# Optimization experiments

Hardware: AMD Instinct MI355X
Metric: run time of the kernel (lower is better)

## Reference

```python
import jax, jax.numpy as jnp
import numpy as np

H, W = 16, 16
DIM = 512
HEADS = 8
DIM_HEAD = 64
INNER = HEADS * DIM_HEAD  # 512
B = 8
N = H * W  # 256
SCALE = DIM_HEAD ** -0.5
EPS = 1e-5


def _index_map(h, w):
    # index_map[n, m] = dx * (2w-1) + dy with dx = x-i+h-1, dy = y-j+w-1
    xs = np.arange(h)
    ys = np.arange(w)
    dx = xs[:, None] - xs[None, :] + h - 1            # (h, h)
    dy = ys[:, None] - ys[None, :] + w - 1            # (w, w)
    idx = dx[:, None, :, None] * (2 * w - 1) + dy[None, :, None, :]  # (h, w, h, w)
    return idx.reshape(h * w, h * w).astype(np.int32)


def setup_inputs() -> dict:
    key = jax.random.key(0)
    ks = jax.random.split(key, 5)
    x = jax.random.normal(ks[0], (B, N, DIM), dtype=jnp.float32)
    ln_g = jnp.ones((DIM,), jnp.float32)
    ln_b = jnp.zeros((DIM,), jnp.float32)
    w_qkv = jax.random.normal(ks[1], (DIM, 3 * INNER), jnp.float32) * 0.02
    unique_params = jax.random.normal(ks[2], ((2 * H - 1) * (2 * W - 1), INNER), jnp.float32) * 0.02
    w_out = jax.random.normal(ks[3], (INNER, DIM), jnp.float32) * 0.02
    b_out = jnp.zeros((DIM,), jnp.float32)
    idx_map = jnp.asarray(_index_map(H, W))  # (N, N) int32
    return {"x": x, "ln_g": ln_g, "ln_b": ln_b, "w_qkv": w_qkv,
            "unique_params": unique_params, "w_out": w_out, "b_out": b_out,
            "idx_map": idx_map}


def reference(x, ln_g, ln_b, w_qkv, unique_params, w_out, b_out, idx_map):
    b, n, _ = x.shape
    # LayerNorm
    mu = jnp.mean(x, axis=-1, keepdims=True)
    var = jnp.mean(jnp.square(x - mu), axis=-1, keepdims=True)
    xn = (x - mu) * jax.lax.rsqrt(var + EPS) * ln_g + ln_b
    # qkv projection (no bias)
    qkv = xn @ w_qkv                                  # (b, n, 3*inner)
    q, k, v = jnp.split(qkv, 3, axis=-1)
    q = q.reshape(b, n, HEADS, DIM_HEAD)
    k = k.reshape(b, n, HEADS, DIM_HEAD)
    v = v.reshape(b, n, HEADS, DIM_HEAD)
    # attention scores
    dots = jnp.einsum('bnhd,bmhd->bhnm', q, k) * SCALE
    attn = jax.nn.softmax(dots, axis=-1)              # (b, h, n, m)
    # relative-position table: (n, m, h, d)
    rpos = unique_params[idx_map].reshape(n, n, HEADS, DIM_HEAD)
    # out[b,h,n,d] = sum_m attn[b,h,n,m] * (v[b,m,h,d] + rpos[n,m,h,d])
    out = jnp.einsum('bhnm,bmhd->bnhd', attn, v) \
        + jnp.einsum('bhnm,nmhd->bnhd', attn, rpos)
    out = out.reshape(b, n, INNER)
    return out @ w_out + b_out
```

## Files before the change

kernel.cpp:

```cpp
#include <hip/hip_runtime.h>
#include <math.h>

#define NB 8
#define SEQ 256
#define DIMC 512
#define NHEAD 8
#define DHEAD 64
#define SCALEF 0.125f

typedef __attribute__((ext_vector_type(8))) short s16x8;
typedef __attribute__((ext_vector_type(4))) float f32x4;

typedef __attribute__((address_space(3))) unsigned int lds_u32_t;
typedef const __attribute__((address_space(1))) unsigned int g_u32_t;
static __device__ __forceinline__ void gl_lds16(const void* gsrc, void* ldst) {
  __builtin_amdgcn_global_load_lds((g_u32_t*)gsrc, (lds_u32_t*)ldst, 16, 0, 0);
}

static __device__ __forceinline__ unsigned short f2bf(float f) {
  union { float f; unsigned u; } c; c.f = f;
  unsigned r = c.u + 0x7FFF + ((c.u >> 16) & 1);
  return (unsigned short)(r >> 16);
}
static __device__ __forceinline__ float bf2f(unsigned short u) {
  union { unsigned u; float f; } c; c.u = ((unsigned)u) << 16;
  return c.f;
}

static __device__ void tcast_body(const float* __restrict__ W,
    unsigned short* __restrict__ WT, int K, int N, int n0, int k0, int t,
    float (*tile)[65]) {
#pragma unroll
  for (int i = 0; i < 16; ++i) {
    const int idx = i * 256 + t;
    const int kl = idx >> 6, nl = idx & 63;
    tile[kl][nl] = W[(size_t)(k0 + kl) * N + n0 + nl];
  }
  __syncthreads();
#pragma unroll
  for (int i = 0; i < 16; ++i) {
    const int idx = i * 256 + t;
    const int nl = idx >> 6, kl = idx & 63;
    WT[(size_t)(n0 + nl) * K + k0 + kl] = f2bf(tile[kl][nl]);
  }
}

__global__ __launch_bounds__(256) void prep_kernel(const float* __restrict__ x,
    const float* __restrict__ g, const float* __restrict__ bta,
    const float* __restrict__ w_qkv, const float* __restrict__ w_out,
    const float* __restrict__ up, unsigned short* __restrict__ xnb,
    unsigned short* __restrict__ wqt, unsigned short* __restrict__ wot,
    unsigned short* __restrict__ upb) {
  __shared__ float tile[64][65];
  __shared__ float sh_s[4], sh_q[4];
  const int t = threadIdx.x;
  const int bid = blockIdx.x;
  if (bid < 192) {
    tcast_body(w_qkv, wqt, 512, 1536, (bid % 24) * 64, (bid / 24) * 64, t, tile);
  } else if (bid < 256) {
    const int b2 = bid - 192;
    tcast_body(w_out, wot, 512, 512, (b2 % 8) * 64, (b2 / 8) * 64, t, tile);
  } else if (bid < 497) {
    const int base = (bid - 256) * 2048 + t * 4;
#pragma unroll
    for (int it = 0; it < 2; ++it) {
      const int i = base + it * 1024;
      if (i < 492032) {
        const float4 v = *(const float4*)&up[i];
        ushort4 w;
        w.x = f2bf(v.x); w.y = f2bf(v.y); w.z = f2bf(v.z); w.w = f2bf(v.w);
        *(ushort4*)&upb[i] = w;
      }
    }
  } else {
    const int row = bid - 497;
    const float2 v = ((const float2*)(x + (size_t)row * DIMC))[t];
    float s = v.x + v.y;
    float q = v.x * v.x + v.y * v.y;
#pragma unroll
    for (int off = 32; off > 0; off >>= 1) {
      s += __shfl_down(s, off);
      q += __shfl_down(q, off);
    }
    const int wave = t >> 6, lane = t & 63;
    if (lane == 0) { sh_s[wave] = s; sh_q[wave] = q; }
    __syncthreads();
    const float fs = sh_s[0] + sh_s[1] + sh_s[2] + sh_s[3];
    const float fq = sh_q[0] + sh_q[1] + sh_q[2] + sh_q[3];
    const float mean = fs * (1.0f / DIMC);
    const float inv = rsqrtf(fq * (1.0f / DIMC) - mean * mean + 1e-5f);
    const float2 gv = ((const float2*)g)[t];
    const float2 bv = ((const float2*)bta)[t];
    ushort2 o;
    o.x = f2bf((v.x - mean) * inv * gv.x + bv.x);
    o.y = f2bf((v.y - mean) * inv * gv.y + bv.y);
    ((ushort2*)(xnb + (size_t)row * DIMC))[t] = o;
  }
}

template <int BM, int BN, bool BIAS, bool OUTBF, bool VSPLIT>
__global__ __launch_bounds__(256) void mfma_gemm_bt(
    const unsigned short* __restrict__ A, const unsigned short* __restrict__ BT,
    const float* __restrict__ bias, void* __restrict__ Cv,
    unsigned short* __restrict__ vtb, int M, int K, int N) {
  constexpr int TR = BM / 32;
  constexpr int TC = BN / 32;
  __shared__ unsigned short As[BM * 32];
  __shared__ unsigned short Bs[BN * 32];
  const int t = threadIdx.x;
  const int wave = t >> 6, lane = t & 63;
  const int wr = wave >> 1, wc = wave & 1;
  const int bm = blockIdx.x * BM, bn = blockIdx.y * BN;

  f32x4 acc[TR][TC] = {};

  const int fr = lane & 15, q4 = lane >> 4;
  const int kBlocks = K >> 5;
  for (int kb = 0; kb < kBlocks; ++kb) {
    const int k0 = kb << 5;
    __syncthreads();
#pragma unroll
    for (int c = 0; c < (BM * 4 + 255) / 256; ++c) {
      const int p = c * 256 + t;
      if (BM * 4 % 256 == 0 || p < BM * 4) {
        const int row = p >> 2;
        const int jl = (p & 3) ^ ((row >> 1) & 3);
        gl_lds16(A + (size_t)(bm + row) * K + k0 + jl * 8,
                 As + (size_t)(c * 256 + wave * 64) * 8);
      }
    }
#pragma unroll
    for (int c = 0; c < (BN * 4 + 255) / 256; ++c) {
      const int p = c * 256 + t;
      if (BN * 4 % 256 == 0 || p < BN * 4) {
        const int row = p >> 2;
        const int jl = (p & 3) ^ ((row >> 1) & 3);
        gl_lds16(BT + (size_t)(bn + row) * K + k0 + jl * 8,
                 Bs + (size_t)(c * 256 + wave * 64) * 8);
      }
    }
    __syncthreads();
    s16x8 af[TR], bfr[TC];
#pragma unroll
    for (int i = 0; i < TR; ++i) {
      const int row = wr * (BM / 2) + i * 16 + fr;
      const int jp = q4 ^ ((row >> 1) & 3);
      af[i] = *(const s16x8*)(As + row * 32 + jp * 8);
    }
#pragma unroll
    for (int j = 0; j < TC; ++j) {
      const int row = wc * (BN / 2) + j * 16 + fr;
      const int jp = q4 ^ ((row >> 1) & 3);
      bfr[j] = *(const s16x8*)(Bs + row * 32 + jp * 8);
    }
#pragma unroll
    for (int i = 0; i < TR; ++i)
#pragma unroll
      for (int j = 0; j < TC; ++j)
        acc[i][j] = __builtin_amdgcn_mfma_f32_16x16x32_bf16(af[i], bfr[j],
                                                            acc[i][j], 0, 0, 0);
  }
  if (VSPLIT && bn >= 1024) {
#pragma unroll
    for (int i = 0; i < TR; ++i) {
#pragma unroll
      for (int j = 0; j < TC; ++j) {
        const int hc = bn - 1024 + wc * (BN / 2) + j * 16 + fr;
        const int h = hc >> 6, d = hc & 63;
#pragma unroll
        for (int r = 0; r < 4; ++r) {
          const int row = bm + wr * (BM / 2) + i * 16 + q4 * 4 + r;
          const int b = row >> 8, m = row & 255;
          vtb[(size_t)((b * 8 + h) * 64 + d) * 256 + m] = f2bf(acc[i][j][r]);
        }
      }
    }
    return;
  }
#pragma unroll
  for (int i = 0; i < TR; ++i) {
#pragma unroll
    for (int j = 0; j < TC; ++j) {
      const int col = bn + wc * (BN / 2) + j * 16 + fr;
      const float bv = BIAS ? bias[col] : 0.0f;
#pragma unroll
      for (int r = 0; r < 4; ++r) {
        const int row = bm + wr * (BM / 2) + i * 16 + q4 * 4 + r;
        if constexpr (OUTBF) {
          ((unsigned short*)Cv)[(size_t)row * N + col] = f2bf(acc[i][j][r] + bv);
        } else {
          ((float*)Cv)[(size_t)row * N + col] = acc[i][j][r] + bv;
        }
      }
    }
  }
}

#define PSTR 264
#define KSTR 72
__global__ __launch_bounds__(128) void fused_attn_kernel(
    const unsigned short* __restrict__ qkvb, const unsigned short* __restrict__ vtb,
    unsigned short* __restrict__ attnb, unsigned short* __restrict__ oav) {
  __shared__ unsigned short kv_lds[256 * KSTR];
  __shared__ unsigned short p_lds[32 * PSTR];
  const int bh = blockIdx.y, b = bh >> 3, h = bh & 7;
  const int n0 = blockIdx.x * 32;
  const int t = threadIdx.x, wave = t >> 6, lane = t & 63;
  const int fr = lane & 15, q4 = lane >> 4;

#pragma unroll
  for (int p = 0; p < 16; ++p) {
    const int chunk = p * 128 + t;
    const int m = chunk >> 3, c = chunk & 7;
    *(s16x8*)(kv_lds + m * KSTR + c * 8) =
        *(const s16x8*)(qkvb + (size_t)(b * SEQ + m) * 1536 + 512 + h * 64 + c * 8);
  }
  s16x8 qf[2];
  {
    const size_t qrow = (size_t)(b * SEQ + n0 + wave * 16 + fr) * 1536 + h * 64;
#pragma unroll
    for (int ks = 0; ks < 2; ++ks)
      qf[ks] = *(const s16x8*)(qkvb + qrow + ks * 32 + q4 * 8);
  }
  __syncthreads();

  f32x4 s[16];
#pragma unroll
  for (int mt = 0; mt < 16; ++mt) s[mt] = (f32x4){0.f, 0.f, 0.f, 0.f};
#pragma unroll
  for (int ks = 0; ks < 2; ++ks)
#pragma unroll
    for (int mt = 0; mt < 16; ++mt) {
      const s16x8 kf =
          *(const s16x8*)(kv_lds + (mt * 16 + fr) * KSTR + ks * 32 + q4 * 8);
      s[mt] = __builtin_amdgcn_mfma_f32_16x16x32_bf16(qf[ks], kf, s[mt], 0, 0, 0);
    }

  float mx[4] = {-1e30f, -1e30f, -1e30f, -1e30f};
#pragma unroll
  for (int mt = 0; mt < 16; ++mt)
#pragma unroll
    for (int r = 0; r < 4; ++r) {
      s[mt][r] *= SCALEF;
      mx[r] = fmaxf(mx[r], s[mt][r]);
    }
#pragma unroll
  for (int r = 0; r < 4; ++r) {
    mx[r] = fmaxf(mx[r], __shfl_xor(mx[r], 1));
    mx[r] = fmaxf(mx[r], __shfl_xor(mx[r], 2));
    mx[r] = fmaxf(mx[r], __shfl_xor(mx[r], 4));
    mx[r] = fmaxf(mx[r], __shfl_xor(mx[r], 8));
  }
  float sum[4] = {0.f, 0.f, 0.f, 0.f};
#pragma unroll
  for (int mt = 0; mt < 16; ++mt)
#pragma unroll
    for (int r = 0; r < 4; ++r) {
      s[mt][r] = __expf(s[mt][r] - mx[r]);
      sum[r] += s[mt][r];
    }
#pragma unroll
  for (int r = 0; r < 4; ++r) {
    sum[r] += __shfl_xor(sum[r], 1);
    sum[r] += __shfl_xor(sum[r], 2);
    sum[r] += __shfl_xor(sum[r], 4);
    sum[r] += __shfl_xor(sum[r], 8);
  }
  const float invs[4] = {1.0f / sum[0], 1.0f / sum[1], 1.0f / sum[2],
                         1.0f / sum[3]};

  __syncthreads();

  {
    const int nb = wave * 16 + q4 * 4;
#pragma unroll
    for (int mt = 0; mt < 16; ++mt)
#pragma unroll
      for (int r = 0; r < 4; ++r)
        p_lds[(nb + r) * PSTR + mt * 16 + fr] = f2bf(s[mt][r] * invs[r]);
  }
#pragma unroll
  for (int p = 0; p < 16; ++p) {
    const int idx = p * 128 + t;
    const int d = idx >> 5, c = idx & 31;
    *(s16x8*)(kv_lds + d * PSTR + c * 8) =
        *(const s16x8*)(vtb + (size_t)(bh * 64 + d) * 256 + c * 8);
  }
  __syncthreads();

#pragma unroll
  for (int p = 0; p < 8; ++p) {
    const int idx = p * 128 + t;
    const int row = idx >> 5, mc = (idx & 31) * 8;
    *(s16x8*)(attnb + (size_t)(bh * SEQ + n0 + row) * SEQ + mc) =
        *(const s16x8*)(p_lds + row * PSTR + mc);
  }

  f32x4 o[4];
#pragma unroll
  for (int dt = 0; dt < 4; ++dt) o[dt] = (f32x4){0.f, 0.f, 0.f, 0.f};
#pragma unroll
  for (int ks = 0; ks < 8; ++ks) {
    const s16x8 pf =
        *(const s16x8*)(p_lds + (wave * 16 + fr) * PSTR + ks * 32 + q4 * 8);
#pragma unroll
    for (int dt = 0; dt < 4; ++dt) {
      const s16x8 vf =
          *(const s16x8*)(kv_lds + (dt * 16 + fr) * PSTR + ks * 32 + q4 * 8);
      o[dt] = __builtin_amdgcn_mfma_f32_16x16x32_bf16(pf, vf, o[dt], 0, 0, 0);
    }
  }
#pragma unroll
  for (int dt = 0; dt < 4; ++dt)
#pragma unroll
    for (int r = 0; r < 4; ++r) {
      const int n = n0 + wave * 16 + q4 * 4 + r;
      oav[(size_t)(b * SEQ + n) * DIMC + h * 64 + dt * 16 + fr] = f2bf(o[dt][r]);
    }
}

#define RSTRIDE 280
__global__ __launch_bounds__(256) void rpos_kernel(
    const unsigned short* __restrict__ attnb, const unsigned short* __restrict__ upb,
    unsigned short* __restrict__ ob) {
  __shared__ float aS[4][4 * RSTRIDE];
  const int t = threadIdx.x;
  const int wave = t >> 6, lane = t & 63;
  const int g = lane >> 4, dg = lane & 15;
  const int idx = blockIdx.x * 4 + wave;
  const int bhalf = idx & 1;
  const int h = (idx >> 1) & 7;
  const int n = idx >> 4;
  float* aW = aS[wave];

  const int m4 = lane * 4;
  const int sm4 = m4 + ((m4 >> 6) << 3);
#pragma unroll
  for (int bl = 0; bl < 4; ++bl) {
    const int b = bhalf * 4 + bl;
    const ushort4 v =
        *(const ushort4*)&attnb[(size_t)((b * 8 + h) * SEQ + n) * SEQ + m4];
    float4 f;
    f.x = bf2f(v.x); f.y = bf2f(v.y); f.z = bf2f(v.z); f.w = bf2f(v.w);
    *(float4*)&aW[bl * RSTRIDE + sm4] = f;
  }
  __syncthreads();

  const int xn = n >> 4, yn = n & 15;
  float acc[4][4];
#pragma unroll
  for (int bl = 0; bl < 4; ++bl)
#pragma unroll
    for (int j = 0; j < 4; ++j) acc[bl][j] = 0.0f;

  const int mbase = g * 64;
  const int sbase = g * 72;
#pragma unroll 4
  for (int mm = 0; mm < 64; ++mm) {
    const int m = mbase + mm;
    const int xm = m >> 4, ym = m & 15;
    const int row = (xn - xm + 15) * 31 + (yn - ym + 15);
    const ushort4 uu = *(const ushort4*)&upb[(size_t)row * DIMC + h * 64 + dg * 4];
    const float ux = bf2f(uu.x), uy = bf2f(uu.y), uz = bf2f(uu.z), uw = bf2f(uu.w);
    float ab[4];
#pragma unroll
    for (int bl = 0; bl < 4; ++bl) ab[bl] = aW[bl * RSTRIDE + sbase + mm];
#pragma unroll
    for (int bl = 0; bl < 4; ++bl) {
      acc[bl][0] += ab[bl] * ux;
      acc[bl][1] += ab[bl] * uy;
      acc[bl][2] += ab[bl] * uz;
      acc[bl][3] += ab[bl] * uw;
    }
  }
#pragma unroll
  for (int bl = 0; bl < 4; ++bl)
#pragma unroll
    for (int j = 0; j < 4; ++j) {
      float v = acc[bl][j];
      v += __shfl_xor(v, 16);
      v += __shfl_xor(v, 32);
      acc[bl][j] = v;
    }
  {
    const int b = bhalf * 4 + g;
    const size_t base = (size_t)(b * SEQ + n) * DIMC + h * 64 + dg * 4;
    ushort4 pv = *(ushort4*)&ob[base];
    ushort4 w;
    w.x = f2bf(bf2f(pv.x) + acc[g][0]);
    w.y = f2bf(bf2f(pv.y) + acc[g][1]);
    w.z = f2bf(bf2f(pv.z) + acc[g][2]);
    w.w = f2bf(bf2f(pv.w) + acc[g][3]);
    *(ushort4*)&ob[base] = w;
  }
}

extern "C" void kernel_launch(void* const* d_in, const int* in_sizes, int n_in,
                              void* d_out, int out_size, void* d_ws,
                              size_t ws_size, hipStream_t stream) {
  const float* x = (const float*)d_in[0];
  const float* ln_g = (const float*)d_in[1];
  const float* ln_b = (const float*)d_in[2];
  const float* w_qkv = (const float*)d_in[3];
  const float* up = (const float*)d_in[4];
  const float* w_out = (const float*)d_in[5];
  const float* b_out = (const float*)d_in[6];
  float* out = (float*)d_out;

  unsigned short* u = (unsigned short*)d_ws;
  unsigned short* qkvb = u;
  unsigned short* attnb = u + 3145728;
  unsigned short* xnb = u + 7340032;
  unsigned short* ob = u + 8388608;
  unsigned short* wqt = u + 9437184;
  unsigned short* wot = u + 10223616;
  unsigned short* upb = u + 10485760;
  unsigned short* vtb = u + 10977792;
  if (ws_size < (size_t)12026368 * sizeof(unsigned short)) return;

  prep_kernel<<<2545, 256, 0, stream>>>(x, ln_g, ln_b, w_qkv, w_out, up,
                                        xnb, wqt, wot, upb);
  mfma_gemm_bt<64, 64, false, true, true>
      <<<dim3(32, 24), 256, 0, stream>>>(xnb, wqt, nullptr, qkvb, vtb,
                                         2048, 512, 1536);
  fused_attn_kernel<<<dim3(8, 64), 128, 0, stream>>>(qkvb, vtb, attnb, ob);
  rpos_kernel<<<1024, 256, 0, stream>>>(attnb, upb, ob);
  mfma_gemm_bt<64, 32, true, false, false>
      <<<dim3(32, 16), 256, 0, stream>>>(ob, wot, b_out, out, nullptr,
                                         2048, 512, 512);
}
```

Before: 120.5 us.

## Use K=64 GEMM tiles, move w_out/up casts into QKV GEMM tail, widen rpos loads

The GEMM kernel now stages 64-wide K slices with an 8-way XOR swizzle and issues two MFMA k-steps per barrier pair, which halves the number of sync iterations. The w_out transpose-cast and the unique_params bf16 cast move out of the prep kernel into extra tail blocks of the QKV GEMM launch, so they overlap with GEMM work and the prep kernel gets shorter. The rpos kernel loads 8 bf16 values per lane instead of 4, splitting m across 8 groups and adding one more shuffle-reduction step. The costs are more LDS per GEMM block and extra reduction shuffles in rpos.

New measurement: 120.7 us. Within noise of the previous version (+0.2%).

```diff
diff --git a/kernel.cpp b/kernel.cpp
--- a/kernel.cpp
+++ b/kernel.cpp
@@ -47,33 +47,16 @@
 
 __global__ __launch_bounds__(256) void prep_kernel(const float* __restrict__ x,
     const float* __restrict__ g, const float* __restrict__ bta,
-    const float* __restrict__ w_qkv, const float* __restrict__ w_out,
-    const float* __restrict__ up, unsigned short* __restrict__ xnb,
-    unsigned short* __restrict__ wqt, unsigned short* __restrict__ wot,
-    unsigned short* __restrict__ upb) {
+    const float* __restrict__ w_qkv, unsigned short* __restrict__ xnb,
+    unsigned short* __restrict__ wqt) {
   __shared__ float tile[64][65];
   __shared__ float sh_s[4], sh_q[4];
   const int t = threadIdx.x;
   const int bid = blockIdx.x;
   if (bid < 192) {
     tcast_body(w_qkv, wqt, 512, 1536, (bid % 24) * 64, (bid / 24) * 64, t, tile);
-  } else if (bid < 256) {
-    const int b2 = bid - 192;
-    tcast_body(w_out, wot, 512, 512, (b2 % 8) * 64, (b2 / 8) * 64, t, tile);
-  } else if (bid < 497) {
-    const int base = (bid - 256) * 2048 + t * 4;
-#pragma unroll
-    for (int it = 0; it < 2; ++it) {
-      const int i = base + it * 1024;
-      if (i < 492032) {
-        const float4 v = *(const float4*)&up[i];
-        ushort4 w;
-        w.x = f2bf(v.x); w.y = f2bf(v.y); w.z = f2bf(v.z); w.w = f2bf(v.w);
-        *(ushort4*)&upb[i] = w;
-      }
-    }
   } else {
-    const int row = bid - 497;
+    const int row = bid - 192;
     const float2 v = ((const float2*)(x + (size_t)row * DIMC))[t];
     float s = v.x + v.y;
     float q = v.x * v.x + v.y * v.y;
@@ -98,67 +81,100 @@
   }
 }
 
-template <int BM, int BN, bool BIAS, bool OUTBF, bool VSPLIT>
-__global__ __launch_bounds__(256) void mfma_gemm_bt(
+template <int BM, int BN, bool BIAS, bool OUTBF, bool VSPLIT, bool TAIL>
+__global__ __launch_bounds__(256) void gemm64_kernel(
     const unsigned short* __restrict__ A, const unsigned short* __restrict__ BT,
     const float* __restrict__ bias, void* __restrict__ Cv,
-    unsigned short* __restrict__ vtb, int M, int K, int N) {
+    unsigned short* __restrict__ vtb, int M, int K, int N, int nbm,
+    const float* __restrict__ w_out, unsigned short* __restrict__ wot,
+    const float* __restrict__ up, unsigned short* __restrict__ upb) {
+  constexpr int ABYTES = (BM * 64 + BN * 64) * 2;
+  constexpr int LDSZ = TAIL ? (ABYTES > 16640 ? ABYTES : 16640) : ABYTES;
+  __shared__ alignas(16) unsigned char smem[LDSZ];
+  unsigned short* As = (unsigned short*)smem;
+  unsigned short* Bs = As + BM * 64;
+  const int t = threadIdx.x;
+  const int bid = blockIdx.x;
+  const int gemmBlocks = nbm * (N / BN);
+
+  if constexpr (TAIL) {
+    if (bid >= gemmBlocks) {
+      const int b2 = bid - gemmBlocks;
+      if (b2 < 64) {
+        float (*tile)[65] = (float(*)[65])smem;
+        tcast_body(w_out, wot, 512, 512, (b2 % 8) * 64, (b2 / 8) * 64, t, tile);
+      } else {
+        const int base = (b2 - 64) * 2048 + t * 4;
+#pragma unroll
+        for (int it = 0; it < 2; ++it) {
+          const int i = base + it * 1024;
+          if (i < 492032) {
+            const float4 v = *(const float4*)&up[i];
+            ushort4 w;
+            w.x = f2bf(v.x); w.y = f2bf(v.y); w.z = f2bf(v.z); w.w = f2bf(v.w);
+            *(ushort4*)&upb[i] = w;
+          }
+        }
+      }
+      return;
+    }
+  }
+
   constexpr int TR = BM / 32;
   constexpr int TC = BN / 32;
-  __shared__ unsigned short As[BM * 32];
-  __shared__ unsigned short Bs[BN * 32];
-  const int t = threadIdx.x;
   const int wave = t >> 6, lane = t & 63;
   const int wr = wave >> 1, wc = wave & 1;
-  const int bm = blockIdx.x * BM, bn = blockIdx.y * BN;
+  const int bm = (bid % nbm) * BM, bn = (bid / nbm) * BN;
+  const int fr = lane & 15, q4 = lane >> 4;
 
   f32x4 acc[TR][TC] = {};
 
-  const int fr = lane & 15, q4 = lane >> 4;
-  const int kBlocks = K >> 5;
+  const int kBlocks = K >> 6;
   for (int kb = 0; kb < kBlocks; ++kb) {
-    const int k0 = kb << 5;
+    const int k0 = kb << 6;
     __syncthreads();
 #pragma unroll
-    for (int c = 0; c < (BM * 4 + 255) / 256; ++c) {
+    for (int c = 0; c < BM * 8 / 256; ++c) {
       const int p = c * 256 + t;
-      if (BM * 4 % 256 == 0 || p < BM * 4) {
-        const int row = p >> 2;
-        const int jl = (p & 3) ^ ((row >> 1) & 3);
-        gl_lds16(A + (size_t)(bm + row) * K + k0 + jl * 8,
-                 As + (size_t)(c * 256 + wave * 64) * 8);
+      const int row = p >> 3;
+      const int jl = (p & 7) ^ (row & 7);
+      gl_lds16(A + (size_t)(bm + row) * K + k0 + jl * 8,
+               As + (size_t)(c * 256 + wave * 64) * 8);
+    }
+#pragma unroll
+    for (int c = 0; c < BN * 8 / 256; ++c) {
+      const int p = c * 256 + t;
+      const int row = p >> 3;
+      const int jl = (p & 7) ^ (row & 7);
+      gl_lds16(BT + (size_t)(bn + row) * K + k0 + jl * 8,
+               Bs + (size_t)(c * 256 + wave * 64) * 8);
+    }
+    __syncthreads();
+    s16x8 af[TR][2], bfr[TC][2];
+#pragma unroll
+    for (int i = 0; i < TR; ++i)
+#pragma unroll
+      for (int ks = 0; ks < 2; ++ks) {
+        const int row = wr * (BM / 2) + i * 16 + fr;
+        const int jp = (ks * 4 + q4) ^ (fr & 7);
+        af[i][ks] = *(const s16x8*)(As + row * 64 + jp * 8);
       }
-    }
-#pragma unroll
-    for (int c = 0; c < (BN * 4 + 255) / 256; ++c) {
-      const int p = c * 256 + t;
-      if (BN * 4 % 256 == 0 || p < BN * 4) {
-        const int row = p >> 2;
-        const int jl = (p & 3) ^ ((row >> 1) & 3);
-        gl_lds16(BT + (size_t)(bn + row) * K + k0 + jl * 8,
-                 Bs + (size_t)(c * 256 + wave * 64) * 8);
+#pragma unroll
+    for (int j = 0; j < TC; ++j)
+#pragma unroll
+      for (int ks = 0; ks < 2; ++ks) {
+        const int row = wc * (BN / 2) + j * 16 + fr;
+        const int jp = (ks * 4 + q4) ^ (fr & 7);
+        bfr[j][ks] = *(const s16x8*)(Bs + row * 64 + jp * 8);
       }
-    }
-    __syncthreads();
-    s16x8 af[TR], bfr[TC];
-#pragma unroll
-    for (int i = 0; i < TR; ++i) {
-      const int row = wr * (BM / 2) + i * 16 + fr;
-      const int jp = q4 ^ ((row >> 1) & 3);
-      af[i] = *(const s16x8*)(As + row * 32 + jp * 8);
-    }
-#pragma unroll
-    for (int j = 0; j < TC; ++j) {
-      const int row = wc * (BN / 2) + j * 16 + fr;
-      const int jp = q4 ^ ((row >> 1) & 3);
-      bfr[j] = *(const s16x8*)(Bs + row * 32 + jp * 8);
-    }
-#pragma unroll
-    for (int i = 0; i < TR; ++i)
-#pragma unroll
-      for (int j = 0; j < TC; ++j)
-        acc[i][j] = __builtin_amdgcn_mfma_f32_16x16x32_bf16(af[i], bfr[j],
-                                                            acc[i][j], 0, 0, 0);
+#pragma unroll
+    for (int ks = 0; ks < 2; ++ks)
+#pragma unroll
+      for (int i = 0; i < TR; ++i)
+#pragma unroll
+        for (int j = 0; j < TC; ++j)
+          acc[i][j] = __builtin_amdgcn_mfma_f32_16x16x32_bf16(
+              af[i][ks], bfr[j][ks], acc[i][j], 0, 0, 0);
   }
   if (VSPLIT && bn >= 1024) {
 #pragma unroll
@@ -326,7 +342,6 @@
   __shared__ float aS[4][4 * RSTRIDE];
   const int t = threadIdx.x;
   const int wave = t >> 6, lane = t & 63;
-  const int g = lane >> 4, dg = lane & 15;
   const int idx = blockIdx.x * 4 + wave;
   const int bhalf = idx & 1;
   const int h = (idx >> 1) & 7;
@@ -346,52 +361,51 @@
   }
   __syncthreads();
 
+  const int g = lane >> 3, dl = lane & 7;
   const int xn = n >> 4, yn = n & 15;
-  float acc[4][4];
+  float acc[4][8];
 #pragma unroll
   for (int bl = 0; bl < 4; ++bl)
 #pragma unroll
-    for (int j = 0; j < 4; ++j) acc[bl][j] = 0.0f;
-
-  const int mbase = g * 64;
-  const int sbase = g * 72;
+    for (int j = 0; j < 8; ++j) acc[bl][j] = 0.0f;
+
+  const int sbase = g * 32 + (g >> 1) * 8;
 #pragma unroll 4
-  for (int mm = 0; mm < 64; ++mm) {
-    const int m = mbase + mm;
+  for (int mm = 0; mm < 32; ++mm) {
+    const int m = g * 32 + mm;
     const int xm = m >> 4, ym = m & 15;
     const int row = (xn - xm + 15) * 31 + (yn - ym + 15);
-    const ushort4 uu = *(const ushort4*)&upb[(size_t)row * DIMC + h * 64 + dg * 4];
-    const float ux = bf2f(uu.x), uy = bf2f(uu.y), uz = bf2f(uu.z), uw = bf2f(uu.w);
+    const s16x8 uv = *(const s16x8*)(upb + (size_t)row * DIMC + h * 64 + dl * 8);
+    float uf[8];
+#pragma unroll
+    for (int j = 0; j < 8; ++j) uf[j] = bf2f((unsigned short)uv[j]);
     float ab[4];
 #pragma unroll
     for (int bl = 0; bl < 4; ++bl) ab[bl] = aW[bl * RSTRIDE + sbase + mm];
 #pragma unroll
-    for (int bl = 0; bl < 4; ++bl) {
-      acc[bl][0] += ab[bl] * ux;
-      acc[bl][1] += ab[bl] * uy;
-      acc[bl][2] += ab[bl] * uz;
-      acc[bl][3] += ab[bl] * uw;
-    }
+    for (int bl = 0; bl < 4; ++bl)
+#pragma unroll
+      for (int j = 0; j < 8; ++j) acc[bl][j] += ab[bl] * uf[j];
   }
 #pragma unroll
   for (int bl = 0; bl < 4; ++bl)
 #pragma unroll
-    for (int j = 0; j < 4; ++j) {
+    for (int j = 0; j < 8; ++j) {
       float v = acc[bl][j];
+      v += __shfl_xor(v, 8);
       v += __shfl_xor(v, 16);
       v += __shfl_xor(v, 32);
       acc[bl][j] = v;
     }
-  {
+  if (g < 4) {
     const int b = bhalf * 4 + g;
-    const size_t base = (size_t)(b * SEQ + n) * DIMC + h * 64 + dg * 4;
-    ushort4 pv = *(ushort4*)&ob[base];
-    ushort4 w;
-    w.x = f2bf(bf2f(pv.x) + acc[g][0]);
-    w.y = f2bf(bf2f(pv.y) + acc[g][1]);
-    w.z = f2bf(bf2f(pv.z) + acc[g][2]);
-    w.w = f2bf(bf2f(pv.w) + acc[g][3]);
-    *(ushort4*)&ob[base] = w;
+    unsigned short* p = ob + (size_t)(b * SEQ + n) * DIMC + h * 64 + dl * 8;
+    s16x8 pv = *(s16x8*)p;
+    s16x8 w;
+#pragma unroll
+    for (int j = 0; j < 8; ++j)
+      w[j] = (short)f2bf(bf2f((unsigned short)pv[j]) + acc[g][j]);
+    *(s16x8*)p = w;
   }
 }
 
@@ -418,14 +432,13 @@
   unsigned short* vtb = u + 10977792;
   if (ws_size < (size_t)12026368 * sizeof(unsigned short)) return;
 
-  prep_kernel<<<2545, 256, 0, stream>>>(x, ln_g, ln_b, w_qkv, w_out, up,
-                                        xnb, wqt, wot, upb);
-  mfma_gemm_bt<64, 64, false, true, true>
-      <<<dim3(32, 24), 256, 0, stream>>>(xnb, wqt, nullptr, qkvb, vtb,
-                                         2048, 512, 1536);
+  prep_kernel<<<2240, 256, 0, stream>>>(x, ln_g, ln_b, w_qkv, xnb, wqt);
+  gemm64_kernel<64, 64, false, true, true, true>
+      <<<1073, 256, 0, stream>>>(xnb, wqt, nullptr, qkvb, vtb, 2048, 512, 1536,
+                                 32, w_out, wot, up, upb);
   fused_attn_kernel<<<dim3(8, 64), 128, 0, stream>>>(qkvb, vtb, attnb, ob);
   rpos_kernel<<<1024, 256, 0, stream>>>(attnb, upb, ob);
-  mfma_gemm_bt<64, 32, true, false, false>
-      <<<dim3(32, 16), 256, 0, stream>>>(ob, wot, b_out, out, nullptr,
-                                         2048, 512, 512);
-}
+  gemm64_kernel<64, 32, true, false, false, false>
+      <<<512, 256, 0, stream>>>(ob, wot, b_out, out, nullptr, 2048, 512, 512,
+                                32, nullptr, nullptr, nullptr, nullptr);
+}
```
